# Optimization experiments

Hardware: AMD Instinct MI355X
Metric: run time of the kernel (lower is better)

## Reference

```python
import jax, jax.numpy as jnp
import numpy as np

VOCAB = 32000
EMB = 512
HID = 1024
BATCH = 64
SEQ = 64
EPS_THRESHOLD = 0.5  # eps_end + (eps_start-eps_end)*exp(-4*0/decay) with step=0 -> eps_start


def setup_inputs() -> dict:
    key = jax.random.key(0)
    ks = jax.random.split(key, 9)
    s = 0.05  # small init scale for numerical stability
    return {
        'emb': jax.random.normal(ks[0], (VOCAB, EMB), jnp.float32) * s,
        'w_ih': jax.random.normal(ks[1], (3 * HID, EMB), jnp.float32) * s,
        'w_hh': jax.random.normal(ks[2], (3 * HID, HID), jnp.float32) * s,
        'b_ih': jax.random.normal(ks[3], (3 * HID,), jnp.float32) * s,
        'b_hh': jax.random.normal(ks[4], (3 * HID,), jnp.float32) * s,
        'w_out': jax.random.normal(ks[5], (VOCAB, HID), jnp.float32) * s,
        'b_out': jax.random.normal(ks[6], (VOCAB,), jnp.float32) * s,
        'gumbel_u': jax.random.uniform(ks[7], (SEQ, BATCH, VOCAB), jnp.float32),
        'eps_u': jax.random.uniform(ks[8], (SEQ, BATCH), jnp.float32),
    }


def _rollout(emb, w_ih, w_hh, b_ih, b_hh, w_out, b_out, gumbel_u, eps_u):
    log_v = jnp.log(jnp.float32(VOCAB))

    def step(carry, xs):
        h, x = carry            # h: [B,H], x: [B,E]
        gu, eu = xs             # gu: [B,V], eu: [B]
        gi = x @ w_ih.T + b_ih  # [B,3H]
        gh = h @ w_hh.T + b_hh  # [B,3H]
        i_r, i_z, i_n = jnp.split(gi, 3, axis=1)
        h_r, h_z, h_n = jnp.split(gh, 3, axis=1)
        r = jax.nn.sigmoid(i_r + h_r)
        z = jax.nn.sigmoid(i_z + h_z)
        n = jnp.tanh(i_n + r * h_n)
        h_new = (1.0 - z) * n + z * h
        dist = jax.nn.log_softmax(h_new @ w_out.T + b_out, axis=-1)  # [B,V]
        draw = eu <= EPS_THRESHOLD  # eps-greedy rows -> uniform behavioral dist
        behav = jnp.where(draw[:, None], -log_v, dist)
        u = jnp.clip(gu, 1e-12, 1.0 - 1e-12)
        sampled = jnp.argmax(behav - jnp.log(-jnp.log(u)), axis=1)  # Gumbel-max, [B]
        idx = sampled[:, None]
        lp = jnp.take_along_axis(dist, idx, axis=1)[:, 0]            # on-policy logprob
        off = jnp.clip(jnp.exp(jnp.take_along_axis(behav, idx, axis=1)[:, 0]), 0.001, 1.0)
        corr = jnp.exp(jax.lax.stop_gradient(lp)) / off              # importance weight
        return (h_new, emb[sampled]), (sampled, corr, lp)

    h0 = jnp.zeros((BATCH, HID), jnp.float32)
    x0 = jnp.broadcast_to(emb[0], (BATCH, EMB))  # embedding of zero tokens
    _, (outs, corrs, lps) = jax.lax.scan(step, (h0, x0), (gumbel_u, eps_u))
    return outs.T, corrs.T, lps.T  # each [B,S]


def reference(emb, w_ih, w_hh, b_ih, b_hh, w_out, b_out, gumbel_u, eps_u):
    return _rollout(emb, w_ih, w_hh, b_ih, b_hh, w_out, b_out, gumbel_u, eps_u)
```

## Files before the change

kernel.cpp:

```cpp
#include <hip/hip_runtime.h>
#include <math.h>

#define NBATCH 64
#define EMBD   512
#define HIDD   1024
#define NVOC   32000
#define SEQL   64
#define NVT    500


__global__ __launch_bounds__(256) void k_init(const float* __restrict__ emb,
                                              float* __restrict__ ws) {
    int b = blockIdx.x, tid = threadIdx.x;
    float* h0 = ws;
    float* x  = ws + 131072;
    for (int j = tid; j < HIDD; j += 256) h0[b * HIDD + j] = 0.f;
    for (int k = tid; k < EMBD; k += 256) x[b * EMBD + k] = emb[k];
}

__device__ __forceinline__ void gemm_core(const float* __restrict__ W,
                                          const float* __restrict__ X,
                                          int K, int n0,
                                          float (*Ws)[68], float (*Xs)[68],
                                          float acc[4][4]) {
    int tid = threadIdx.x;
    int tx = tid & 15, ty = tid >> 4;
    int ldr = tid >> 2;
    int kq  = (tid & 3) * 4;

    for (int k0 = 0; k0 < K; k0 += 16) {
        float4 w4 = *(const float4*)(W + (size_t)(n0 + ldr) * K + k0 + kq);
        float4 x4 = *(const float4*)(X + (size_t)ldr * K + k0 + kq);
        __syncthreads();
        Ws[kq + 0][ldr] = w4.x; Ws[kq + 1][ldr] = w4.y;
        Ws[kq + 2][ldr] = w4.z; Ws[kq + 3][ldr] = w4.w;
        Xs[kq + 0][ldr] = x4.x; Xs[kq + 1][ldr] = x4.y;
        Xs[kq + 2][ldr] = x4.z; Xs[kq + 3][ldr] = x4.w;
        __syncthreads();
#pragma unroll
        for (int kk = 0; kk < 16; ++kk) {
            float4 a = *(const float4*)&Ws[kk][4 * ty];
            float4 b = *(const float4*)&Xs[kk][4 * tx];
            acc[0][0] += a.x * b.x; acc[0][1] += a.x * b.y;
            acc[0][2] += a.x * b.z; acc[0][3] += a.x * b.w;
            acc[1][0] += a.y * b.x; acc[1][1] += a.y * b.y;
            acc[1][2] += a.y * b.z; acc[1][3] += a.y * b.w;
            acc[2][0] += a.z * b.x; acc[2][1] += a.z * b.y;
            acc[2][2] += a.z * b.z; acc[2][3] += a.z * b.w;
            acc[3][0] += a.w * b.x; acc[3][1] += a.w * b.y;
            acc[3][2] += a.w * b.z; acc[3][3] += a.w * b.w;
        }
    }
}

__global__ __launch_bounds__(256) void k_gates(
    const float* __restrict__ w_ih, const float* __restrict__ b_ih,
    const float* __restrict__ x,    float* __restrict__ gi,
    const float* __restrict__ w_hh, const float* __restrict__ b_hh,
    const float* __restrict__ h,    float* __restrict__ gh) {
    __shared__ float Ws[16][68], Xs[16][68];
    const float* W; const float* X; const float* bias; float* out; int K;
    if (blockIdx.y == 0) { W = w_ih; X = x; bias = b_ih; out = gi; K = EMBD; }
    else                 { W = w_hh; X = h; bias = b_hh; out = gh; K = HIDD; }
    int n0 = blockIdx.x * 64;
    float acc[4][4] = {};
    gemm_core(W, X, K, n0, Ws, Xs, acc);
    int tid = threadIdx.x, tx = tid & 15, ty = tid >> 4;
#pragma unroll
    for (int i = 0; i < 4; ++i) {
        int n = n0 + 4 * ty + i;
        float bi = bias[n];
        float4 o = make_float4(acc[i][0] + bi, acc[i][1] + bi,
                               acc[i][2] + bi, acc[i][3] + bi);
        *(float4*)(out + n * 64 + 4 * tx) = o;
    }
}

__global__ __launch_bounds__(256) void k_gru(
    const float* __restrict__ gi, const float* __restrict__ gh,
    const float* __restrict__ h_in, float* __restrict__ h_out) {
    int tid = blockIdx.x * 256 + threadIdx.x;
    int b = tid & 63, j = tid >> 6;
    float ir = gi[j * 64 + b], iz = gi[(j + 1024) * 64 + b], in_ = gi[(j + 2048) * 64 + b];
    float hr = gh[j * 64 + b], hz = gh[(j + 1024) * 64 + b], hn = gh[(j + 2048) * 64 + b];
    float h = h_in[b * HIDD + j];
    float r = 1.f / (1.f + expf(-(ir + hr)));
    float z = 1.f / (1.f + expf(-(iz + hz)));
    float n = tanhf(in_ + r * hn);
    h_out[b * HIDD + j] = (1.f - z) * n + z * h;
}

__global__ __launch_bounds__(256) void k_logits(
    const float* __restrict__ w_out, const float* __restrict__ b_out,
    const float* __restrict__ h, float* __restrict__ logits,
    float* __restrict__ pm, float* __restrict__ ps) {
    __shared__ float Ws[16][68], Xs[16][68];
    __shared__ float red[16][64];
    __shared__ float sm[64];
    int v0 = blockIdx.x * 64;
    float acc[4][4] = {};
    gemm_core(w_out, h, HIDD, v0, Ws, Xs, acc);
    int tid = threadIdx.x, tx = tid & 15, ty = tid >> 4;
    float val[4][4];
#pragma unroll
    for (int i = 0; i < 4; ++i) {
        float bi = b_out[v0 + 4 * ty + i];
#pragma unroll
        for (int j = 0; j < 4; ++j) val[i][j] = acc[i][j] + bi;
    }
#pragma unroll
    for (int j = 0; j < 4; ++j) {
        float4 o = make_float4(val[0][j], val[1][j], val[2][j], val[3][j]);
        *(float4*)(logits + (size_t)(4 * tx + j) * NVOC + v0 + 4 * ty) = o;
    }
    __syncthreads();
#pragma unroll
    for (int j = 0; j < 4; ++j) {
        float mj = fmaxf(fmaxf(val[0][j], val[1][j]), fmaxf(val[2][j], val[3][j]));
        red[ty][4 * tx + j] = mj;
    }
    __syncthreads();
    if (tid < 64) {
        float m = red[0][tid];
#pragma unroll
        for (int r = 1; r < 16; ++r) m = fmaxf(m, red[r][tid]);
        sm[tid] = m;
    }
    __syncthreads();
#pragma unroll
    for (int j = 0; j < 4; ++j) {
        float mb = sm[4 * tx + j];
        float s = expf(val[0][j] - mb) + expf(val[1][j] - mb) +
                  expf(val[2][j] - mb) + expf(val[3][j] - mb);
        red[ty][4 * tx + j] = s;
    }
    __syncthreads();
    if (tid < 64) {
        float s = 0.f;
#pragma unroll
        for (int r = 0; r < 16; ++r) s += red[r][tid];
        pm[blockIdx.x * 64 + tid] = sm[tid];
        ps[blockIdx.x * 64 + tid] = s;
    }
}

__global__ __launch_bounds__(256) void k_sample(
    const float* __restrict__ logits, const float* __restrict__ pm,
    const float* __restrict__ ps, const float* __restrict__ gumbel,
    const float* __restrict__ eps, const float* __restrict__ emb,
    float* __restrict__ xout, float* __restrict__ out, int t) {
    int b = blockIdx.x, tid = threadIdx.x;
    __shared__ float sred[256];
    __shared__ int sidx[256];

    float m = -INFINITY;
    for (int c = tid; c < NVT; c += 256) m = fmaxf(m, pm[c * 64 + b]);
    sred[tid] = m;
    __syncthreads();
    for (int s = 128; s > 0; s >>= 1) {
        if (tid < s) sred[tid] = fmaxf(sred[tid], sred[tid + s]);
        __syncthreads();
    }
    float M = sred[0];
    __syncthreads();
    float ss = 0.f;
    for (int c = tid; c < NVT; c += 256) ss += ps[c * 64 + b] * expf(pm[c * 64 + b] - M);
    sred[tid] = ss;
    __syncthreads();
    for (int s = 128; s > 0; s >>= 1) {
        if (tid < s) sred[tid] += sred[tid + s];
        __syncthreads();
    }
    float lse = M + logf(sred[0]);
    __syncthreads();

    bool draw = eps[t * 64 + b] <= 0.5f;
    const float LOGV = logf(32000.0f);
    const float* lrow = logits + (size_t)b * NVOC;
    const float* grow = gumbel + ((size_t)t * 64 + b) * NVOC;
    float bestv = -INFINITY; int besti = 0x7fffffff;
    for (int v = tid; v < NVOC; v += 256) {
        float u = grow[v];
        u = fminf(fmaxf(u, 1e-12f), 1.0f);
        float g = -logf(-logf(u));
        float base = draw ? -LOGV : (lrow[v] - lse);
        float sc = base + g;
        if (sc > bestv) { bestv = sc; besti = v; }
    }
    sred[tid] = bestv; sidx[tid] = besti;
    __syncthreads();
    for (int s = 128; s > 0; s >>= 1) {
        if (tid < s) {
            float ov = sred[tid + s]; int oi = sidx[tid + s];
            if (ov > sred[tid] || (ov == sred[tid] && oi < sidx[tid])) {
                sred[tid] = ov; sidx[tid] = oi;
            }
        }
        __syncthreads();
    }
    int sampled = sidx[0];
    if (tid == 0) {
        float lp = lrow[sampled] - lse;
        float bs = draw ? -LOGV : lp;
        float off = fminf(fmaxf(expf(bs), 0.001f), 1.0f);
        float corr = expf(lp) / off;
        out[b * SEQL + t] = (float)sampled;
        out[4096 + b * SEQL + t] = corr;
        out[8192 + b * SEQL + t] = lp;
    }
    const float* erow = emb + (size_t)sampled * EMBD;
    for (int k = tid; k < EMBD; k += 256) xout[b * EMBD + k] = erow[k];
}

extern "C" void kernel_launch(void* const* d_in, const int* in_sizes, int n_in,
                              void* d_out, int out_size, void* d_ws, size_t ws_size,
                              hipStream_t stream) {
    const float* emb   = (const float*)d_in[0];
    const float* w_ih  = (const float*)d_in[1];
    const float* w_hh  = (const float*)d_in[2];
    const float* b_ih  = (const float*)d_in[3];
    const float* b_hh  = (const float*)d_in[4];
    const float* w_out = (const float*)d_in[5];
    const float* b_out = (const float*)d_in[6];
    const float* gum   = (const float*)d_in[7];
    const float* eps   = (const float*)d_in[8];
    float* out = (float*)d_out;
    float* ws  = (float*)d_ws;

    float* h0     = ws;
    float* h1     = ws + 65536;
    float* x      = ws + 131072;
    float* gi     = ws + 163840;
    float* gh     = ws + 360448;
    float* logits = ws + 557056;
    float* pm     = ws + 2605056;
    float* psum   = ws + 2637056;

    k_init<<<64, 256, 0, stream>>>(emb, ws);
    for (int t = 0; t < SEQL; ++t) {
        float* hin  = (t & 1) ? h1 : h0;
        float* hout = (t & 1) ? h0 : h1;
        k_gates<<<dim3(48, 2), 256, 0, stream>>>(w_ih, b_ih, x, gi,
                                                 w_hh, b_hh, hin, gh);
        k_gru<<<256, 256, 0, stream>>>(gi, gh, hin, hout);
        k_logits<<<NVT, 256, 0, stream>>>(w_out, b_out, hout, logits, pm, psum);
        k_sample<<<64, 256, 0, stream>>>(logits, pm, psum, gum, eps, emb, x, out, t);
    }
}
```

Measured before the change: 13.07 ms.

## Fuse Gumbel sampling into logits GEMM and split-K the gate GEMMs

Measured after the change: 28.87 ms. +120.9%, slower.

```diff
diff --git a/kernel.cpp b/kernel.cpp
--- a/kernel.cpp
+++ b/kernel.cpp
@@ -1,12 +1,11 @@
 #include <hip/hip_runtime.h>
 #include <math.h>
 
-#define NBATCH 64
-#define EMBD   512
-#define HIDD   1024
-#define NVOC   32000
-#define SEQL   64
-#define NVT    500
+#define EMBD 512
+#define HIDD 1024
+#define NVOC 32000
+#define SEQL 64
+#define NVT  500
 
 
 __global__ __launch_bounds__(256) void k_init(const float* __restrict__ emb,
@@ -18,71 +17,65 @@
     for (int k = tid; k < EMBD; k += 256) x[b * EMBD + k] = emb[k];
 }
 
-__device__ __forceinline__ void gemm_core(const float* __restrict__ W,
-                                          const float* __restrict__ X,
-                                          int K, int n0,
-                                          float (*Ws)[68], float (*Xs)[68],
-                                          float acc[4][4]) {
-    int tid = threadIdx.x;
-    int tx = tid & 15, ty = tid >> 4;
-    int ldr = tid >> 2;
-    int kq  = (tid & 3) * 4;
-
-    for (int k0 = 0; k0 < K; k0 += 16) {
-        float4 w4 = *(const float4*)(W + (size_t)(n0 + ldr) * K + k0 + kq);
-        float4 x4 = *(const float4*)(X + (size_t)ldr * K + k0 + kq);
-        __syncthreads();
-        Ws[kq + 0][ldr] = w4.x; Ws[kq + 1][ldr] = w4.y;
-        Ws[kq + 2][ldr] = w4.z; Ws[kq + 3][ldr] = w4.w;
-        Xs[kq + 0][ldr] = x4.x; Xs[kq + 1][ldr] = x4.y;
-        Xs[kq + 2][ldr] = x4.z; Xs[kq + 3][ldr] = x4.w;
-        __syncthreads();
-#pragma unroll
-        for (int kk = 0; kk < 16; ++kk) {
-            float4 a = *(const float4*)&Ws[kk][4 * ty];
-            float4 b = *(const float4*)&Xs[kk][4 * tx];
-            acc[0][0] += a.x * b.x; acc[0][1] += a.x * b.y;
-            acc[0][2] += a.x * b.z; acc[0][3] += a.x * b.w;
-            acc[1][0] += a.y * b.x; acc[1][1] += a.y * b.y;
-            acc[1][2] += a.y * b.z; acc[1][3] += a.y * b.w;
-            acc[2][0] += a.z * b.x; acc[2][1] += a.z * b.y;
-            acc[2][2] += a.z * b.z; acc[2][3] += a.z * b.w;
-            acc[3][0] += a.w * b.x; acc[3][1] += a.w * b.y;
-            acc[3][2] += a.w * b.z; acc[3][3] += a.w * b.w;
-        }
-    }
-}
-
 __global__ __launch_bounds__(256) void k_gates(
     const float* __restrict__ w_ih, const float* __restrict__ b_ih,
-    const float* __restrict__ x,    float* __restrict__ gi,
+    const float* __restrict__ xin,
     const float* __restrict__ w_hh, const float* __restrict__ b_hh,
-    const float* __restrict__ h,    float* __restrict__ gh) {
-    __shared__ float Ws[16][68], Xs[16][68];
-    const float* W; const float* X; const float* bias; float* out; int K;
-    if (blockIdx.y == 0) { W = w_ih; X = x; bias = b_ih; out = gi; K = EMBD; }
-    else                 { W = w_hh; X = h; bias = b_hh; out = gh; K = HIDD; }
-    int n0 = blockIdx.x * 64;
-    float acc[4][4] = {};
-    gemm_core(W, X, K, n0, Ws, Xs, acc);
-    int tid = threadIdx.x, tx = tid & 15, ty = tid >> 4;
-#pragma unroll
-    for (int i = 0; i < 4; ++i) {
-        int n = n0 + 4 * ty + i;
-        float bi = bias[n];
-        float4 o = make_float4(acc[i][0] + bi, acc[i][1] + bi,
-                               acc[i][2] + bi, acc[i][3] + bi);
-        *(float4*)(out + n * 64 + 4 * tx) = o;
+    const float* __restrict__ h,
+    float* __restrict__ gi0, float* __restrict__ gi1,
+    float* __restrict__ gh0, float* __restrict__ gh1) {
+    __shared__ float Xs[32][64];
+    int tid = threadIdx.x;
+    int wid = __builtin_amdgcn_readfirstlane(tid >> 6);
+    int lane = tid & 63;
+    int mat = blockIdx.z, kc = blockIdx.y;
+    const float* W    = mat ? w_hh : w_ih;
+    const float* X    = mat ? h    : xin;
+    const float* bias = mat ? b_hh : b_ih;
+    float* out = mat ? (kc ? gh1 : gh0) : (kc ? gi1 : gi0);
+    int K  = mat ? HIDD : EMBD;
+    int Kh = K >> 1;
+    int kbase = kc * Kh;
+    int rbase = blockIdx.x * 64 + wid * 16;
+
+    float acc[16];
+#pragma unroll
+    for (int v = 0; v < 16; ++v) acc[v] = 0.f;
+
+    for (int k0 = 0; k0 < Kh; k0 += 32) {
+        int r = tid >> 2, c = (tid & 3) * 8;
+        const float* hp = X + (size_t)r * K + kbase + k0 + c;
+        float4 a0 = *(const float4*)hp;
+        float4 a1 = *(const float4*)(hp + 4);
+        __syncthreads();
+        Xs[c + 0][r] = a0.x; Xs[c + 1][r] = a0.y; Xs[c + 2][r] = a0.z; Xs[c + 3][r] = a0.w;
+        Xs[c + 4][r] = a1.x; Xs[c + 5][r] = a1.y; Xs[c + 6][r] = a1.z; Xs[c + 7][r] = a1.w;
+        __syncthreads();
+        const float* wb = W + (size_t)rbase * K + kbase + k0;
+#pragma unroll
+        for (int kk = 0; kk < 32; ++kk) {
+            float xk = Xs[kk][lane];
+#pragma unroll
+            for (int v = 0; v < 16; ++v)
+                acc[v] += wb[(size_t)v * K + kk] * xk;
+        }
+    }
+#pragma unroll
+    for (int v = 0; v < 16; ++v) {
+        float o = acc[v] + (kc == 0 ? bias[rbase + v] : 0.f);
+        out[(rbase + v) * 64 + lane] = o;
     }
 }
 
 __global__ __launch_bounds__(256) void k_gru(
-    const float* __restrict__ gi, const float* __restrict__ gh,
+    const float* __restrict__ gi0, const float* __restrict__ gi1,
+    const float* __restrict__ gh0, const float* __restrict__ gh1,
     const float* __restrict__ h_in, float* __restrict__ h_out) {
     int tid = blockIdx.x * 256 + threadIdx.x;
     int b = tid & 63, j = tid >> 6;
-    float ir = gi[j * 64 + b], iz = gi[(j + 1024) * 64 + b], in_ = gi[(j + 2048) * 64 + b];
-    float hr = gh[j * 64 + b], hz = gh[(j + 1024) * 64 + b], hn = gh[(j + 2048) * 64 + b];
+    int i0 = j * 64 + b, i1 = (j + 1024) * 64 + b, i2 = (j + 2048) * 64 + b;
+    float ir = gi0[i0] + gi1[i0], iz = gi0[i1] + gi1[i1], in_ = gi0[i2] + gi1[i2];
+    float hr = gh0[i0] + gh1[i0], hz = gh0[i1] + gh1[i1], hn = gh0[i2] + gh1[i2];
     float h = h_in[b * HIDD + j];
     float r = 1.f / (1.f + expf(-(ir + hr)));
     float z = 1.f / (1.f + expf(-(iz + hz)));
@@ -92,115 +85,141 @@
 
 __global__ __launch_bounds__(256) void k_logits(
     const float* __restrict__ w_out, const float* __restrict__ b_out,
-    const float* __restrict__ h, float* __restrict__ logits,
-    float* __restrict__ pm, float* __restrict__ ps) {
-    __shared__ float Ws[16][68], Xs[16][68];
-    __shared__ float red[16][64];
-    __shared__ float sm[64];
+    const float* __restrict__ h, const float* __restrict__ gum,
+    const float* __restrict__ eps,
+    float* __restrict__ pm, float* __restrict__ ps,
+    float* __restrict__ bv, float* __restrict__ bl, int* __restrict__ bi, int t) {
+    __shared__ float Xs[32][64];
+    __shared__ float rm[4][64], rs[4][64], rv[4][64], rl[4][64];
+    __shared__ int   ri[4][64];
+    int tid = threadIdx.x;
+    int wid = __builtin_amdgcn_readfirstlane(tid >> 6);
+    int lane = tid & 63;
     int v0 = blockIdx.x * 64;
-    float acc[4][4] = {};
-    gemm_core(w_out, h, HIDD, v0, Ws, Xs, acc);
-    int tid = threadIdx.x, tx = tid & 15, ty = tid >> 4;
-    float val[4][4];
-#pragma unroll
-    for (int i = 0; i < 4; ++i) {
-        float bi = b_out[v0 + 4 * ty + i];
-#pragma unroll
-        for (int j = 0; j < 4; ++j) val[i][j] = acc[i][j] + bi;
-    }
-#pragma unroll
-    for (int j = 0; j < 4; ++j) {
-        float4 o = make_float4(val[0][j], val[1][j], val[2][j], val[3][j]);
-        *(float4*)(logits + (size_t)(4 * tx + j) * NVOC + v0 + 4 * ty) = o;
-    }
-    __syncthreads();
-#pragma unroll
-    for (int j = 0; j < 4; ++j) {
-        float mj = fmaxf(fmaxf(val[0][j], val[1][j]), fmaxf(val[2][j], val[3][j]));
-        red[ty][4 * tx + j] = mj;
-    }
-    __syncthreads();
-    if (tid < 64) {
-        float m = red[0][tid];
-#pragma unroll
-        for (int r = 1; r < 16; ++r) m = fmaxf(m, red[r][tid]);
-        sm[tid] = m;
-    }
-    __syncthreads();
-#pragma unroll
-    for (int j = 0; j < 4; ++j) {
-        float mb = sm[4 * tx + j];
-        float s = expf(val[0][j] - mb) + expf(val[1][j] - mb) +
-                  expf(val[2][j] - mb) + expf(val[3][j] - mb);
-        red[ty][4 * tx + j] = s;
-    }
-    __syncthreads();
-    if (tid < 64) {
-        float s = 0.f;
-#pragma unroll
-        for (int r = 0; r < 16; ++r) s += red[r][tid];
-        pm[blockIdx.x * 64 + tid] = sm[tid];
-        ps[blockIdx.x * 64 + tid] = s;
-    }
-}
-
-__global__ __launch_bounds__(256) void k_sample(
-    const float* __restrict__ logits, const float* __restrict__ pm,
-    const float* __restrict__ ps, const float* __restrict__ gumbel,
-    const float* __restrict__ eps, const float* __restrict__ emb,
-    float* __restrict__ xout, float* __restrict__ out, int t) {
-    int b = blockIdx.x, tid = threadIdx.x;
-    __shared__ float sred[256];
-    __shared__ int sidx[256];
-
-    float m = -INFINITY;
-    for (int c = tid; c < NVT; c += 256) m = fmaxf(m, pm[c * 64 + b]);
-    sred[tid] = m;
-    __syncthreads();
-    for (int s = 128; s > 0; s >>= 1) {
-        if (tid < s) sred[tid] = fmaxf(sred[tid], sred[tid + s]);
-        __syncthreads();
-    }
-    float M = sred[0];
-    __syncthreads();
-    float ss = 0.f;
-    for (int c = tid; c < NVT; c += 256) ss += ps[c * 64 + b] * expf(pm[c * 64 + b] - M);
-    sred[tid] = ss;
-    __syncthreads();
-    for (int s = 128; s > 0; s >>= 1) {
-        if (tid < s) sred[tid] += sred[tid + s];
-        __syncthreads();
-    }
-    float lse = M + logf(sred[0]);
-    __syncthreads();
-
-    bool draw = eps[t * 64 + b] <= 0.5f;
+    int rbase = v0 + wid * 16;
+
+    float acc[16];
+#pragma unroll
+    for (int v = 0; v < 16; ++v) acc[v] = 0.f;
+
+    for (int k0 = 0; k0 < HIDD; k0 += 32) {
+        int r = tid >> 2, c = (tid & 3) * 8;
+        const float* hp = h + (size_t)r * HIDD + k0 + c;
+        float4 a0 = *(const float4*)hp;
+        float4 a1 = *(const float4*)(hp + 4);
+        __syncthreads();
+        Xs[c + 0][r] = a0.x; Xs[c + 1][r] = a0.y; Xs[c + 2][r] = a0.z; Xs[c + 3][r] = a0.w;
+        Xs[c + 4][r] = a1.x; Xs[c + 5][r] = a1.y; Xs[c + 6][r] = a1.z; Xs[c + 7][r] = a1.w;
+        __syncthreads();
+        const float* wb = w_out + (size_t)rbase * HIDD + k0;
+#pragma unroll
+        for (int kk = 0; kk < 32; ++kk) {
+            float xk = Xs[kk][lane];
+#pragma unroll
+            for (int v = 0; v < 16; ++v)
+                acc[v] += wb[(size_t)v * HIDD + kk] * xk;
+        }
+    }
+
+    float lv[16];
+#pragma unroll
+    for (int v = 0; v < 16; ++v) lv[v] = acc[v] + b_out[rbase + v];
+    float m = lv[0];
+#pragma unroll
+    for (int v = 1; v < 16; ++v) m = fmaxf(m, lv[v]);
+    float s = 0.f;
+#pragma unroll
+    for (int v = 0; v < 16; ++v) s += expf(lv[v] - m);
+
+    bool draw = eps[t * 64 + lane] <= 0.5f;
     const float LOGV = logf(32000.0f);
-    const float* lrow = logits + (size_t)b * NVOC;
-    const float* grow = gumbel + ((size_t)t * 64 + b) * NVOC;
-    float bestv = -INFINITY; int besti = 0x7fffffff;
-    for (int v = tid; v < NVOC; v += 256) {
+    const float* grow = gum + ((size_t)t * 64 + lane) * NVOC + rbase;
+    float bestv = -INFINITY, bestl = 0.f; int besti = 0x7fffffff;
+#pragma unroll
+    for (int v = 0; v < 16; ++v) {
         float u = grow[v];
         u = fminf(fmaxf(u, 1e-12f), 1.0f);
         float g = -logf(-logf(u));
-        float base = draw ? -LOGV : (lrow[v] - lse);
-        float sc = base + g;
-        if (sc > bestv) { bestv = sc; besti = v; }
-    }
-    sred[tid] = bestv; sidx[tid] = besti;
-    __syncthreads();
-    for (int s = 128; s > 0; s >>= 1) {
-        if (tid < s) {
-            float ov = sred[tid + s]; int oi = sidx[tid + s];
-            if (ov > sred[tid] || (ov == sred[tid] && oi < sidx[tid])) {
-                sred[tid] = ov; sidx[tid] = oi;
+        float sc = (draw ? -LOGV : lv[v]) + g;
+        if (sc > bestv) { bestv = sc; besti = rbase + v; bestl = lv[v]; }
+    }
+
+    rm[wid][lane] = m; rs[wid][lane] = s; rv[wid][lane] = bestv;
+    rl[wid][lane] = bestl; ri[wid][lane] = besti;
+    __syncthreads();
+    if (tid < 64) {
+        int b = tid;
+        float M = rm[0][b];
+#pragma unroll
+        for (int w = 1; w < 4; ++w) M = fmaxf(M, rm[w][b]);
+        float S = 0.f;
+#pragma unroll
+        for (int w = 0; w < 4; ++w) S += rs[w][b] * expf(rm[w][b] - M);
+        float BV = rv[0][b], BL = rl[0][b]; int BI = ri[0][b];
+#pragma unroll
+        for (int w = 1; w < 4; ++w) {
+            float ov = rv[w][b]; int oi = ri[w][b];
+            if (ov > BV || (ov == BV && oi < BI)) { BV = ov; BI = oi; BL = rl[w][b]; }
+        }
+        int o = blockIdx.x * 64 + b;
+        pm[o] = M; ps[o] = S; bv[o] = BV; bl[o] = BL; bi[o] = BI;
+    }
+}
+
+__global__ __launch_bounds__(256) void k_final(
+    const float* __restrict__ pm, const float* __restrict__ ps,
+    const float* __restrict__ bv, const float* __restrict__ bl,
+    const int* __restrict__ bi, const float* __restrict__ eps,
+    const float* __restrict__ emb,
+    float* __restrict__ xout, float* __restrict__ out, int t) {
+    int b = blockIdx.x, tid = threadIdx.x;
+    __shared__ float sr[256], sv[256], sl[256];
+    __shared__ int   si[256];
+    __shared__ int   s_samp;
+
+    float M = -INFINITY;
+    for (int c = tid; c < NVT; c += 256) M = fmaxf(M, pm[c * 64 + b]);
+    sr[tid] = M;
+    __syncthreads();
+    for (int st = 128; st > 0; st >>= 1) {
+        if (tid < st) sr[tid] = fmaxf(sr[tid], sr[tid + st]);
+        __syncthreads();
+    }
+    M = sr[0];
+    __syncthreads();
+    float S = 0.f;
+    for (int c = tid; c < NVT; c += 256) S += ps[c * 64 + b] * expf(pm[c * 64 + b] - M);
+    sr[tid] = S;
+    __syncthreads();
+    for (int st = 128; st > 0; st >>= 1) {
+        if (tid < st) sr[tid] += sr[tid + st];
+        __syncthreads();
+    }
+    float lse = M + logf(sr[0]);
+    __syncthreads();
+
+    float BV = -INFINITY, BL = 0.f; int BI = 0x7fffffff;
+    for (int c = tid; c < NVT; c += 256) {
+        float ov = bv[c * 64 + b]; int oi = bi[c * 64 + b];
+        if (ov > BV || (ov == BV && oi < BI)) { BV = ov; BI = oi; BL = bl[c * 64 + b]; }
+    }
+    sv[tid] = BV; si[tid] = BI; sl[tid] = BL;
+    __syncthreads();
+    for (int st = 128; st > 0; st >>= 1) {
+        if (tid < st) {
+            float ov = sv[tid + st]; int oi = si[tid + st];
+            if (ov > sv[tid] || (ov == sv[tid] && oi < si[tid])) {
+                sv[tid] = ov; si[tid] = oi; sl[tid] = sl[tid + st];
             }
         }
         __syncthreads();
     }
-    int sampled = sidx[0];
     if (tid == 0) {
-        float lp = lrow[sampled] - lse;
+        int sampled = si[0];
+        s_samp = sampled;
+        float lp = sl[0] - lse;
+        bool draw = eps[t * 64 + b] <= 0.5f;
+        const float LOGV = logf(32000.0f);
         float bs = draw ? -LOGV : lp;
         float off = fminf(fmaxf(expf(bs), 0.001f), 1.0f);
         float corr = expf(lp) / off;
@@ -208,7 +227,8 @@
         out[4096 + b * SEQL + t] = corr;
         out[8192 + b * SEQL + t] = lp;
     }
-    const float* erow = emb + (size_t)sampled * EMBD;
+    __syncthreads();
+    const float* erow = emb + (size_t)s_samp * EMBD;
     for (int k = tid; k < EMBD; k += 256) xout[b * EMBD + k] = erow[k];
 }
 
@@ -227,23 +247,28 @@
     float* out = (float*)d_out;
     float* ws  = (float*)d_ws;
 
-    float* h0     = ws;
-    float* h1     = ws + 65536;
-    float* x      = ws + 131072;
-    float* gi     = ws + 163840;
-    float* gh     = ws + 360448;
-    float* logits = ws + 557056;
-    float* pm     = ws + 2605056;
-    float* psum   = ws + 2637056;
+    float* h0  = ws;
+    float* h1  = ws + 65536;
+    float* x   = ws + 131072;
+    float* gi0 = ws + 163840;
+    float* gi1 = ws + 360448;
+    float* gh0 = ws + 557056;
+    float* gh1 = ws + 753664;
+    float* pm  = ws + 950272;
+    float* psm = ws + 982272;
+    float* bv  = ws + 1014272;
+    float* bl  = ws + 1046272;
+    int*   bi  = (int*)(ws + 1078272);
 
     k_init<<<64, 256, 0, stream>>>(emb, ws);
     for (int t = 0; t < SEQL; ++t) {
         float* hin  = (t & 1) ? h1 : h0;
         float* hout = (t & 1) ? h0 : h1;
-        k_gates<<<dim3(48, 2), 256, 0, stream>>>(w_ih, b_ih, x, gi,
-                                                 w_hh, b_hh, hin, gh);
-        k_gru<<<256, 256, 0, stream>>>(gi, gh, hin, hout);
-        k_logits<<<NVT, 256, 0, stream>>>(w_out, b_out, hout, logits, pm, psum);
-        k_sample<<<64, 256, 0, stream>>>(logits, pm, psum, gum, eps, emb, x, out, t);
-    }
-}
+        k_gates<<<dim3(48, 2, 2), 256, 0, stream>>>(w_ih, b_ih, x, w_hh, b_hh, hin,
+                                                    gi0, gi1, gh0, gh1);
+        k_gru<<<256, 256, 0, stream>>>(gi0, gi1, gh0, gh1, hin, hout);
+        k_logits<<<NVT, 256, 0, stream>>>(w_out, b_out, hout, gum, eps,
+                                          pm, psm, bv, bl, bi, t);
+        k_final<<<64, 256, 0, stream>>>(pm, psm, bv, bl, bi, eps, emb, x, out, t);
+    }
+}
```
